# Performance work log

Measured on AMD Instinct MI355X. Metric: run time of the kernel, lower is better.

## Reference

```python
import jax, jax.numpy as jnp
import numpy as np

NA = 100000   # authors
NP_ = 100000  # papers
D = 128       # hidden dim
H = 4         # heads
DH = 32       # head dim (D = H*DH)
L = 2         # layers
R = 3         # relations: 0=writes(a->p), 1=rev_writes(p->a), 2=cites(p->p)
E = 400000    # edges per relation
OUT = 40


def setup_inputs() -> dict:
    key = jax.random.key(0)
    ks = jax.random.split(key, 16)
    s = 0.05
    return {
        "x_author": jax.random.normal(ks[0], (NA, D), jnp.float32),
        "x_paper": jax.random.normal(ks[1], (NP_, D), jnp.float32),
        "ei_writes": jax.random.randint(ks[2], (2, E), 0, NA, dtype=jnp.int32),
        "ei_rev": jax.random.randint(ks[3], (2, E), 0, NA, dtype=jnp.int32),
        "ei_cites": jax.random.randint(ks[4], (2, E), 0, NP_, dtype=jnp.int32),
        "proj_w": jax.random.normal(ks[5], (2, D, D), jnp.float32) * s,
        "proj_b": jax.random.normal(ks[6], (2, D), jnp.float32) * s,
        "kqv_w": jax.random.normal(ks[7], (L, 3, 2, D, D), jnp.float32) * s,  # [layer, {k,q,v}, type, D, D]
        "kqv_b": jax.random.normal(ks[8], (L, 3, 2, D), jnp.float32) * s,
        "out_w": jax.random.normal(ks[9], (L, 2, D, D), jnp.float32) * s,
        "out_b": jax.random.normal(ks[10], (L, 2, D), jnp.float32) * s,
        "rel_a": jax.random.normal(ks[11], (L, R, H, DH, DH), jnp.float32) * s,
        "rel_m": jax.random.normal(ks[12], (L, R, H, DH, DH), jnp.float32) * s,
        "p_rel": jnp.ones((L, R, H), jnp.float32),
        "skip": jnp.ones((L, 2), jnp.float32),
        "cls_w": jax.random.normal(ks[13], (D, OUT), jnp.float32) * s,
        "cls_b": jnp.zeros((OUT,), jnp.float32),
    }


def _seg_softmax(sc, dst, n):
    # softmax over incoming edges grouped by destination node; sc: [E,H]
    m = jax.ops.segment_max(sc, dst, num_segments=n)
    m = jnp.where(jnp.isfinite(m), m, 0.0)
    e = jnp.exp(sc - m[dst])
    z = jax.ops.segment_sum(e, dst, num_segments=n)
    return e / (z[dst] + 1e-16)


def _hgt_layer(h_a, h_p, ei_w, ei_r, ei_c, kqv_w, kqv_b, out_w, out_b, rel_a, rel_m, p_rel, skip):
    na, npp = h_a.shape[0], h_p.shape[0]

    def kqv(h, t):
        k = (h @ kqv_w[0, t] + kqv_b[0, t]).reshape(-1, H, DH)
        q = (h @ kqv_w[1, t] + kqv_b[1, t]).reshape(-1, H, DH)
        v = (h @ kqv_w[2, t] + kqv_b[2, t]).reshape(-1, H, DH)
        return k, q, v

    k_a, q_a, v_a = kqv(h_a, 0)
    k_p, q_p, v_p = kqv(h_p, 1)
    scale = 1.0 / jnp.sqrt(jnp.float32(DH))

    def edge_msgs(k_src, v_src, q_dst, ei, r):
        ke = jnp.einsum('ehd,hdf->ehf', k_src[ei[0]], rel_a[r])
        ve = jnp.einsum('ehd,hdf->ehf', v_src[ei[0]], rel_m[r])
        sc = (q_dst[ei[1]] * ke).sum(-1) * p_rel[r] * scale  # [E,H]
        return sc, ve

    # destination = paper: writes (r=0) + cites (r=2); softmax jointly per dst node
    sc_w, ve_w = edge_msgs(k_a, v_a, q_p, ei_w, 0)
    sc_c, ve_c = edge_msgs(k_p, v_p, q_p, ei_c, 2)
    sc_p = jnp.concatenate([sc_w, sc_c], 0)
    ve_p = jnp.concatenate([ve_w, ve_c], 0)
    dst_p = jnp.concatenate([ei_w[1], ei_c[1]], 0)
    al_p = _seg_softmax(sc_p, dst_p, npp)
    agg_p = jax.ops.segment_sum(ve_p * al_p[..., None], dst_p, num_segments=npp).reshape(npp, D)

    # destination = author: rev_writes (r=1)
    sc_r, ve_r = edge_msgs(k_p, v_p, q_a, ei_r, 1)
    al_a = _seg_softmax(sc_r, ei_r[1], na)
    agg_a = jax.ops.segment_sum(ve_r * al_a[..., None], ei_r[1], num_segments=na).reshape(na, D)

    def out_mix(agg, h, t):
        o = jax.nn.gelu(agg, approximate=False) @ out_w[t] + out_b[t]
        s = jax.nn.sigmoid(skip[t])
        return s * o + (1.0 - s) * h

    # HGTNet.forward applies ELU after each HGTConv (dropout is identity in eval mode)
    h_a = jax.nn.elu(out_mix(agg_a, h_a, 0))
    h_p = jax.nn.elu(out_mix(agg_p, h_p, 1))
    return h_a, h_p


def reference(x_author, x_paper, ei_writes, ei_rev, ei_cites, proj_w, proj_b,
              kqv_w, kqv_b, out_w, out_b, rel_a, rel_m, p_rel, skip, cls_w, cls_b):
    h_a = x_author @ proj_w[0] + proj_b[0]
    h_p = x_paper @ proj_w[1] + proj_b[1]
    for l in range(L):
        h_a, h_p = _hgt_layer(h_a, h_p, ei_writes, ei_rev, ei_cites,
                              kqv_w[l], kqv_b[l], out_w[l], out_b[l],
                              rel_a[l], rel_m[l], p_rel[l], skip[l])
    return h_p @ cls_w + cls_b
```

## Files before the change

### kernel.cpp

```cpp
#include <hip/hip_runtime.h>
#include <hip/hip_bf16.h>
#include <math.h>

constexpr int NA  = 100000;
constexpr int NPP = 100000;
constexpr int D   = 128;
constexpr int H   = 4;
constexpr int E   = 400000;
constexpr int R   = 3;
constexpr int L   = 2;
constexpr int NSLOT = 23;
constexpr int SLOT_ELEMS = 8 * 4 * 512;
constexpr int GB2c = (NA + 127) / 128;
constexpr int GAc  = NA / 8;
constexpr int MEGA_G = 1564 * 9;

using s8v = __attribute__((ext_vector_type(8))) short;
using f4v = __attribute__((ext_vector_type(4))) float;
typedef unsigned short ushort_t;

static __device__ __forceinline__ unsigned short f2bf(float f) {
  unsigned u = __float_as_uint(f);
  return (unsigned short)((u + 0x7fffu + ((u >> 16) & 1u)) >> 16);
}
static __device__ __forceinline__ float bf2f(unsigned short s) {
  return __uint_as_float(((unsigned)s) << 16);
}
static __device__ __forceinline__ float klo(int i) {
  return __uint_as_float(((unsigned)i) << 16);
}
static __device__ __forceinline__ float vhi(int i) {
  return __uint_as_float(((unsigned)i) & 0xffff0000u);
}
static __device__ __forceinline__ float gelu_f(float x) {
  return 0.5f * x * (1.0f + erff(x * 0.70710678118654752f));
}
static __device__ __forceinline__ float elu_f(float x) {
  return x > 0.0f ? x : expm1f(x);
}

static __device__ __forceinline__ void load_a2(
    const ushort_t* __restrict__ A, int ar0, int ar1, int ks, int g,
    s8v& a0, s8v& a1) {
  const ushort_t* ap0 = A + (size_t)ar0 * 128 + ks * 32 + g * 4;
  ushort4 u0 = *(const ushort4*)ap0;
  ushort4 u1 = *(const ushort4*)(ap0 + 16);
  a0[0]=(short)u0.x; a0[1]=(short)u0.y; a0[2]=(short)u0.z; a0[3]=(short)u0.w;
  a0[4]=(short)u1.x; a0[5]=(short)u1.y; a0[6]=(short)u1.z; a0[7]=(short)u1.w;
  const ushort_t* ap1 = A + (size_t)ar1 * 128 + ks * 32 + g * 4;
  ushort4 v0 = *(const ushort4*)ap1;
  ushort4 v1 = *(const ushort4*)(ap1 + 16);
  a1[0]=(short)v0.x; a1[1]=(short)v0.y; a1[2]=(short)v0.z; a1[3]=(short)v0.w;
  a1[4]=(short)v1.x; a1[5]=(short)v1.y; a1[6]=(short)v1.z; a1[7]=(short)v1.w;
}

template<bool GELU_A, bool MIX>
__device__ __forceinline__ void dev_gemm8(
    const ushort_t* __restrict__ A, const ushort_t* __restrict__ Bhi,
    const float* __restrict__ bias, ushort_t* __restrict__ Cout,
    const float* __restrict__ skip_ptr, int M, int bx, ushort_t* Bs) {
  for (int i = threadIdx.x; i < 2048; i += 256)
    *(s8v*)&Bs[i * 8] = *(const s8v*)(Bhi + (size_t)i * 8);
  __syncthreads();
  const int lane = threadIdx.x & 63;
  const int wave = threadIdx.x >> 6;
  const int row0 = bx * 128 + wave * 32;
  const int g = lane >> 4, li = lane & 15;
  f4v acc0[8], acc1[8];
#pragma unroll
  for (int ct = 0; ct < 8; ++ct) {
    acc0[ct] = f4v{0.f, 0.f, 0.f, 0.f};
    acc1[ct] = f4v{0.f, 0.f, 0.f, 0.f};
  }
  int ar0 = row0 + li;       if (ar0 >= M) ar0 = M - 1;
  int ar1 = row0 + 16 + li;  if (ar1 >= M) ar1 = M - 1;
#pragma unroll
  for (int ks = 0; ks < 4; ++ks) {
    s8v a0, a1;
    load_a2(A, ar0, ar1, ks, g, a0, a1);
    if (GELU_A) {
#pragma unroll
      for (int i = 0; i < 8; ++i) {
        a0[i] = (short)f2bf(gelu_f(bf2f((unsigned short)a0[i])));
        a1[i] = (short)f2bf(gelu_f(bf2f((unsigned short)a1[i])));
      }
    }
#pragma unroll
    for (int ct = 0; ct < 8; ++ct) {
      s8v bhi = *(const s8v*)&Bs[(ct * 4 + ks) * 512 + lane * 8];
      acc0[ct] = __builtin_amdgcn_mfma_f32_16x16x32_bf16(a0, bhi, acc0[ct], 0, 0, 0);
      acc1[ct] = __builtin_amdgcn_mfma_f32_16x16x32_bf16(a1, bhi, acc1[ct], 0, 0, 0);
    }
  }
  float sskip = 0.f;
  if (MIX) sskip = 1.f / (1.f + __expf(-*skip_ptr));
#pragma unroll
  for (int rf = 0; rf < 2; ++rf) {
#pragma unroll
    for (int ct = 0; ct < 8; ++ct) {
      int col = ct * 16 + li;
      float bv = bias[col];
      f4v a = rf ? acc1[ct] : acc0[ct];
#pragma unroll
      for (int r = 0; r < 4; ++r) {
        int grow = row0 + rf * 16 + g * 4 + r;
        if (grow < M) {
          float v = a[r] + bv;
          size_t off = (size_t)grow * 128 + col;
          if constexpr (MIX) {
            float hprev = bf2f(Cout[off]);
            Cout[off] = f2bf(elu_f(sskip * v + (1.f - sskip) * hprev));
          } else {
            Cout[off] = f2bf(v);
          }
        }
      }
    }
  }
}

__device__ __forceinline__ void dev_gemm_kv(
    const ushort_t* __restrict__ A, const ushort_t* __restrict__ Bkv,
    const float* __restrict__ bias, ushort_t* __restrict__ kvout,
    int M, int bx, int ch, ushort_t* Bs) {
  for (int i = threadIdx.x; i < 2048; i += 256) {
    int kvh = i >> 10, j = i & 1023;
    const ushort_t* src = Bkv + (size_t)kvh * SLOT_ELEMS + ch * 8192 + j * 8;
    *(s8v*)&Bs[kvh * 8192 + j * 8] = *(const s8v*)src;
  }
  __syncthreads();
  const int lane = threadIdx.x & 63;
  const int wave = threadIdx.x >> 6;
  const int row0 = bx * 128 + wave * 32;
  const int g = lane >> 4, li = lane & 15;
  f4v acc0[8], acc1[8];
#pragma unroll
  for (int t = 0; t < 8; ++t) {
    acc0[t] = f4v{0.f, 0.f, 0.f, 0.f};
    acc1[t] = f4v{0.f, 0.f, 0.f, 0.f};
  }
  int ar0 = row0 + li;       if (ar0 >= M) ar0 = M - 1;
  int ar1 = row0 + 16 + li;  if (ar1 >= M) ar1 = M - 1;
#pragma unroll
  for (int ks = 0; ks < 4; ++ks) {
    s8v a0, a1;
    load_a2(A, ar0, ar1, ks, g, a0, a1);
#pragma unroll
    for (int t = 0; t < 4; ++t) {
      s8v kh = *(const s8v*)&Bs[(t * 4 + ks) * 512 + lane * 8];
      acc0[t] = __builtin_amdgcn_mfma_f32_16x16x32_bf16(a0, kh, acc0[t], 0, 0, 0);
      acc1[t] = __builtin_amdgcn_mfma_f32_16x16x32_bf16(a1, kh, acc1[t], 0, 0, 0);
      s8v vh = *(const s8v*)&Bs[8192 + (t * 4 + ks) * 512 + lane * 8];
      acc0[4 + t] = __builtin_amdgcn_mfma_f32_16x16x32_bf16(a0, vh, acc0[4 + t], 0, 0, 0);
      acc1[4 + t] = __builtin_amdgcn_mfma_f32_16x16x32_bf16(a1, vh, acc1[4 + t], 0, 0, 0);
    }
  }
#pragma unroll
  for (int rf = 0; rf < 2; ++rf) {
#pragma unroll
    for (int t = 0; t < 4; ++t) {
      int col = ch * 64 + t * 16 + li;
      float bk = bias[col], bv = bias[128 + col];
#pragma unroll
      for (int r = 0; r < 4; ++r) {
        int grow = row0 + rf * 16 + g * 4 + r;
        if (grow < M) {
          float kvl = rf ? acc1[t][r] : acc0[t][r];
          float vvl = rf ? acc1[4 + t][r] : acc0[4 + t][r];
          ushort2 o;
          o.x = f2bf(kvl + bk);
          o.y = f2bf(vvl + bv);
          *(ushort2*)(kvout + (size_t)grow * 256 + 2 * col) = o;
        }
      }
    }
  }
}

template<bool TWO>
__device__ __forceinline__ void dev_attn(
    const int* __restrict__ rp1, const int* __restrict__ col1,
    const ushort_t* __restrict__ kv1,
    const int* __restrict__ rp2, const int* __restrict__ col2,
    const ushort_t* __restrict__ kv2,
    const ushort_t* __restrict__ q,
    const float* __restrict__ prel1, const float* __restrict__ prel2,
    ushort_t* __restrict__ aggout, int ablk) {
  int lane = threadIdx.x & 63;
  int wave = threadIdx.x >> 6;
  int half = lane >> 5;
  int l32  = lane & 31;
  int dst  = ablk * 8 + wave * 2 + half;
  int head = l32 >> 3;
  const float scale = 0.17677669529663688f;
  float pr1 = prel1[head] * scale;
  float pr2 = TWO ? prel2[head] * scale : pr1;
  ushort4 qv = *(const ushort4*)(q + (size_t)dst * D + l32 * 4);
  float q0 = bf2f(qv.x), q1 = bf2f(qv.y), q2 = bf2f(qv.z), q3 = bf2f(qv.w);
  int e0a = rp1[dst];
  int d1  = rp1[dst + 1] - e0a;
  int e0b = 0, dt = d1;
  if (TWO) { e0b = rp2[dst]; dt = d1 + (rp2[dst + 1] - e0b); }
  float z = 0.f, a0 = 0.f, a1 = 0.f, a2 = 0.f, a3 = 0.f;
  for (int jj = 0; jj < dt; jj += 4) {
    int4 us[4]; bool vs[4]; float prs[4];
#pragma unroll
    for (int s2 = 0; s2 < 4; ++s2) {
      int idx = jj + s2;
      bool v = idx < dt;
      bool f = (!TWO) || (idx < d1);
      int ci = 0;
      if (v) ci = f ? (e0a + idx) : (e0b + idx - d1);
      int src = f ? col1[ci] : col2[ci];
      const ushort_t* kvp = f ? kv1 : kv2;
      us[s2] = *(const int4*)(kvp + (size_t)src * 256 + l32 * 8);
      vs[s2] = v;
      prs[s2] = f ? pr1 : pr2;
    }
#pragma unroll
    for (int s2 = 0; s2 < 4; ++s2) {
      float p = q0 * klo(us[s2].x) + q1 * klo(us[s2].y)
              + q2 * klo(us[s2].z) + q3 * klo(us[s2].w);
      p += __shfl_xor(p, 1);
      p += __shfl_xor(p, 2);
      p += __shfl_xor(p, 4);
      float e = vs[s2] ? __expf(p * prs[s2]) : 0.f;
      z  += e;
      a0 += e * vhi(us[s2].x);
      a1 += e * vhi(us[s2].y);
      a2 += e * vhi(us[s2].z);
      a3 += e * vhi(us[s2].w);
    }
  }
  float inv = 1.f / (z + 1e-16f);
  ushort4 o;
  o.x = f2bf(a0 * inv);
  o.y = f2bf(a1 * inv);
  o.z = f2bf(a2 * inv);
  o.w = f2bf(a3 * inv);
  *(ushort4*)(aggout + (size_t)dst * D + l32 * 4) = o;
}

__global__ __launch_bounds__(256, 8) void attn_p(
    const int* __restrict__ rp1, const int* __restrict__ col1,
    const ushort_t* __restrict__ kv1,
    const int* __restrict__ rp2, const int* __restrict__ col2,
    const ushort_t* __restrict__ kv2,
    const ushort_t* __restrict__ q,
    const float* __restrict__ prel1, const float* __restrict__ prel2,
    ushort_t* __restrict__ aggout) {
  dev_attn<true>(rp1, col1, kv1, rp2, col2, kv2, q, prel1, prel2, aggout, blockIdx.x);
}

__global__ __launch_bounds__(256, 4) void mega0(
    const int* __restrict__ rp_r, const int* __restrict__ col_r,
    const ushort_t* __restrict__ kv1, const ushort_t* __restrict__ q,
    const float* __restrict__ prelR, ushort_t* __restrict__ aggout,
    const ushort_t* __restrict__ h_a, const ushort_t* __restrict__ Bkv0,
    const float* __restrict__ cb0, ushort_t* __restrict__ kv2out) {
  __shared__ ushort_t Bs[16384];
  unsigned gidx = blockIdx.x;
  if (gidx % 9 == 0) {
    int gb = gidx / 9;
    dev_gemm_kv(h_a, Bkv0, cb0, kv2out, NA, gb >> 1, gb & 1, Bs);
  } else {
    int ablk = gidx - gidx / 9 - 1;
    if (ablk < GAc)
      dev_attn<false>(rp_r, col_r, kv1, nullptr, nullptr, nullptr,
                      q, prelR, prelR, aggout, ablk);
  }
}

__global__ __launch_bounds__(256, 4) void fusedA(
    const ushort_t* __restrict__ agg_a, const ushort_t* __restrict__ Bout,
    const float* __restrict__ out_b0, ushort_t* __restrict__ h_a,
    const float* __restrict__ skip0,
    const ushort_t* __restrict__ h_p, const ushort_t* __restrict__ Bq,
    const float* __restrict__ bq_p, ushort_t* __restrict__ qout,
    const ushort_t* __restrict__ Bkv, const float* __restrict__ cb2,
    ushort_t* __restrict__ kvout) {
  __shared__ ushort_t Bs[16384];
  if (blockIdx.y == 0) {
    dev_gemm8<true, true>(agg_a, Bout, out_b0, h_a, skip0, NA, blockIdx.x, Bs);
  } else if (blockIdx.y == 1) {
    dev_gemm8<false, false>(h_p, Bq, bq_p, qout, nullptr, NPP, blockIdx.x, Bs);
  } else {
    dev_gemm_kv(h_p, Bkv, cb2, kvout, NPP, blockIdx.x, blockIdx.y - 2, Bs);
  }
}

__global__ __launch_bounds__(256, 4) void gemm_qkv(
    const ushort_t* __restrict__ Aq, const ushort_t* __restrict__ Akv,
    const ushort_t* __restrict__ Bq, const ushort_t* __restrict__ Bkv,
    const float* __restrict__ bias_q, const float* __restrict__ bias_kv,
    ushort_t* __restrict__ qout, ushort_t* __restrict__ kvout, int M) {
  __shared__ ushort_t Bs[16384];
  if (blockIdx.y == 0)
    dev_gemm8<false, false>(Aq, Bq, bias_q, qout, nullptr, M, blockIdx.x, Bs);
  else
    dev_gemm_kv(Akv, Bkv, bias_kv, kvout, M, blockIdx.x, blockIdx.y - 1, Bs);
}

__global__ __launch_bounds__(256, 4) void outmix(
    const ushort_t* __restrict__ agg, const ushort_t* __restrict__ Bout,
    const float* __restrict__ out_b1, ushort_t* __restrict__ h,
    const float* __restrict__ skip1, int M) {
  __shared__ ushort_t Bs[16384];
  dev_gemm8<true, true>(agg, Bout, out_b1, h, skip1, M, blockIdx.x, Bs);
}

template<int NT16, int NCOLS, int STORE, bool BLO, typename TA>
__global__ __launch_bounds__(256, 4) void gemm4(
    const TA* __restrict__ A,
    const ushort_t* __restrict__ Bhi, const ushort_t* __restrict__ Blo,
    const float* __restrict__ bias, void* __restrict__ Cv, int M) {
  constexpr int HN = NT16 * 2048;
  __shared__ ushort_t Bs[HN * (BLO ? 2 : 1)];
  constexpr bool AFP32 = sizeof(TA) == 4;
  for (int i = threadIdx.x; i < (HN / 8) * (BLO ? 2 : 1); i += 256) {
    int half = i / (HN / 8), j = i % (HN / 8);
    const ushort_t* src = (half ? Blo : Bhi) + (size_t)j * 8;
    *(s8v*)&Bs[half * HN + j * 8] = *(const s8v*)src;
  }
  __syncthreads();
  const int lane = threadIdx.x & 63;
  const int wave = threadIdx.x >> 6;
  const int row0 = blockIdx.x * 128 + wave * 32;
  const int g = lane >> 4, li = lane & 15;
  f4v acc0[NT16], acc1[NT16];
#pragma unroll
  for (int ct = 0; ct < NT16; ++ct) {
    acc0[ct] = f4v{0.f, 0.f, 0.f, 0.f};
    acc1[ct] = f4v{0.f, 0.f, 0.f, 0.f};
  }
  int ar0 = row0 + li;       if (ar0 >= M) ar0 = M - 1;
  int ar1 = row0 + 16 + li;  if (ar1 >= M) ar1 = M - 1;
#pragma unroll
  for (int ks = 0; ks < 4; ++ks) {
    s8v ahi[2], alo[2];
#pragma unroll
    for (int rf = 0; rf < 2; ++rf) {
      int ar = rf ? ar1 : ar0;
      if constexpr (AFP32) {
        const float* ap = (const float*)A + (size_t)ar * 128 + ks * 32 + g * 4;
        float4 u0 = *(const float4*)ap;
        float4 u1 = *(const float4*)(ap + 16);
        float x[8] = {u0.x, u0.y, u0.z, u0.w, u1.x, u1.y, u1.z, u1.w};
#pragma unroll
        for (int i = 0; i < 8; ++i) {
          unsigned short h = f2bf(x[i]);
          ahi[rf][i] = (short)h;
          alo[rf][i] = (short)f2bf(x[i] - bf2f(h));
        }
      } else {
        const ushort_t* ap = (const ushort_t*)A + (size_t)ar * 128 + ks * 32 + g * 4;
        ushort4 u0 = *(const ushort4*)ap;
        ushort4 u1 = *(const ushort4*)(ap + 16);
        ahi[rf][0]=(short)u0.x; ahi[rf][1]=(short)u0.y; ahi[rf][2]=(short)u0.z; ahi[rf][3]=(short)u0.w;
        ahi[rf][4]=(short)u1.x; ahi[rf][5]=(short)u1.y; ahi[rf][6]=(short)u1.z; ahi[rf][7]=(short)u1.w;
      }
    }
#pragma unroll
    for (int ct = 0; ct < NT16; ++ct) {
      const ushort_t* bp = &Bs[(ct * 4 + ks) * 512 + lane * 8];
      s8v bhi = *(const s8v*)bp;
      acc0[ct] = __builtin_amdgcn_mfma_f32_16x16x32_bf16(ahi[0], bhi, acc0[ct], 0, 0, 0);
      acc1[ct] = __builtin_amdgcn_mfma_f32_16x16x32_bf16(ahi[1], bhi, acc1[ct], 0, 0, 0);
      if constexpr (BLO) {
        s8v blo = *(const s8v*)(bp + HN);
        if constexpr (AFP32) {
          acc0[ct] = __builtin_amdgcn_mfma_f32_16x16x32_bf16(alo[0], bhi, acc0[ct], 0, 0, 0);
          acc1[ct] = __builtin_amdgcn_mfma_f32_16x16x32_bf16(alo[1], bhi, acc1[ct], 0, 0, 0);
        }
        acc0[ct] = __builtin_amdgcn_mfma_f32_16x16x32_bf16(ahi[0], blo, acc0[ct], 0, 0, 0);
        acc1[ct] = __builtin_amdgcn_mfma_f32_16x16x32_bf16(ahi[1], blo, acc1[ct], 0, 0, 0);
      }
    }
  }
#pragma unroll
  for (int rf = 0; rf < 2; ++rf) {
#pragma unroll
    for (int ct = 0; ct < NT16; ++ct) {
      int col = ct * 16 + li;
      bool colok = (col < NCOLS);
      float bv = colok ? bias[col] : 0.f;
      f4v a = rf ? acc1[ct] : acc0[ct];
#pragma unroll
      for (int r = 0; r < 4; ++r) {
        int grow = row0 + rf * 16 + g * 4 + r;
        if (grow < M && colok) {
          float v = a[r] + bv;
          size_t off = (size_t)grow * NCOLS + col;
          if constexpr (STORE == 1) ((ushort_t*)Cv)[off] = f2bf(v);
          else                      ((float*)Cv)[off] = v;
        }
      }
    }
  }
}

__global__ __launch_bounds__(256) void combine_w(
    const float* __restrict__ kqv_w, const float* __restrict__ kqv_b,
    const float* __restrict__ rel_a, const float* __restrict__ rel_m,
    float* __restrict__ cw, float* __restrict__ cb) {
  int b  = blockIdx.x;
  int kv = b & 1;
  int r  = (b >> 1) % R;
  int l  = b / (2 * R);
  int t_src = (r == 0) ? 0 : 1;
  int i_w   = (kv == 0) ? 0 : 2;
  const float* W    = kqv_w + ((size_t)((l*3 + i_w)*2 + t_src)) * D * D;
  const float* bvec = kqv_b + ((size_t)((l*3 + i_w)*2 + t_src)) * D;
  const float* rel  = ((kv == 0) ? rel_a : rel_m) + ((size_t)(l*R + r)) * H * 32 * 32;
  float* Cout = cw + (size_t)b * D * D;
  float* cbo  = cb + (size_t)b * D;
  for (int idx = threadIdx.x; idx < D * D; idx += 256) {
    int i = idx / D, j = idx % D;
    int h = j >> 5, f = j & 31;
    const float* relh = rel + h * 32 * 32;
    float sum = 0.f;
#pragma unroll
    for (int d = 0; d < 32; ++d) sum += W[i*D + (h*32 + d)] * relh[d*32 + f];
    Cout[idx] = sum;
  }
  if (threadIdx.x < D) {
    int j = threadIdx.x;
    int h = j >> 5, f = j & 31;
    const float* relh = rel + h * 32 * 32;
    float sum = 0.f;
#pragma unroll
    for (int d = 0; d < 32; ++d) sum += bvec[h*32 + d] * relh[d*32 + f];
    cbo[j] = sum;
  }
}

__global__ __launch_bounds__(256) void pack_b(
    const float* __restrict__ proj_w, const float* __restrict__ kqv_w,
    const float* __restrict__ out_w, const float* __restrict__ cls_w,
    const float* __restrict__ cw,
    ushort_t* __restrict__ phi, ushort_t* __restrict__ plo) {
  int slot = blockIdx.x;
  const float* src; int ncol = 128;
  if (slot == 0) src = proj_w;
  else if (slot == 1) src = proj_w + D * D;
  else if (slot == 22) { src = cls_w; ncol = 40; }
  else {
    int l = (slot - 2) / 10, k = (slot - 2) % 10;
    if (k == 0)      src = kqv_w + ((size_t)((l*3 + 1)*2 + 0)) * D * D;
    else if (k == 1) src = kqv_w + ((size_t)((l*3 + 1)*2 + 1)) * D * D;
    else if (k < 8)  { int idx = k - 2; src = cw + ((size_t)((l*R)*2 + idx)) * D * D; }
    else             src = out_w + ((size_t)(l*2 + (k - 8))) * D * D;
  }
  int nt = (ncol + 15) / 16;
  int total = nt * 4 * 512;
  ushort_t* ph = phi + (size_t)slot * SLOT_ELEMS;
  ushort_t* pl = plo + (size_t)slot * SLOT_ELEMS;
  for (int idx = threadIdx.x; idx < total; idx += 256) {
    int j = idx & 7, lane = (idx >> 3) & 63, ks = (idx >> 9) & 3, ct = idx >> 11;
    int k = 4 * (lane >> 4) + (j & 3) + 16 * (j >> 2) + 32 * ks;
    int n = ct * 16 + (lane & 15);
    float v = (n < ncol) ? src[(size_t)k * ncol + n] : 0.f;
    unsigned short h = f2bf(v);
    ph[idx] = h;
    pl[idx] = f2bf(v - bf2f(h));
  }
}

__global__ void count3(const int* __restrict__ ei_w, const int* __restrict__ ei_c,
                       const int* __restrict__ ei_r, int* __restrict__ degz) {
  const int* dst = blockIdx.y == 0 ? ei_w + E : blockIdx.y == 1 ? ei_c + E : ei_r + E;
  int* deg = degz + blockIdx.y * NPP;
  for (int e = blockIdx.x * blockDim.x + threadIdx.x; e < E; e += gridDim.x * blockDim.x)
    atomicAdd(&deg[dst[e]], 1);
}
__global__ void fill3(const int* __restrict__ ei_w, const int* __restrict__ ei_c,
                      const int* __restrict__ ei_r,
                      const int* __restrict__ rp_w, const int* __restrict__ rp_c,
                      const int* __restrict__ rp_r,
                      int* __restrict__ cntz, int* __restrict__ colz) {
  int rel = blockIdx.y;
  const int* ei = rel == 0 ? ei_w : rel == 1 ? ei_c : ei_r;
  const int* dst = ei + E;
  const int* rp  = rel == 0 ? rp_w : rel == 1 ? rp_c : rp_r;
  int* cnt = cntz + rel * NPP;
  int* col = colz + rel * E;
  for (int e = blockIdx.x * blockDim.x + threadIdx.x; e < E; e += gridDim.x * blockDim.x) {
    int d = dst[e];
    int pos = atomicAdd(&cnt[d], 1);
    col[rp[d] + pos] = ei[e];
  }
}

__global__ __launch_bounds__(256) void scan_partial(const int* __restrict__ degz,
                                                    int* __restrict__ bsum) {
  int blk = blockIdx.x, rel = blk / 25, t25 = blk % 25;
  const int* deg = degz + rel * NPP + t25 * 4096;
  int nrem = min(4096, NPP - t25 * 4096);
  int base = threadIdx.x * 16;
  int s = 0;
  if (base < nrem) {
#pragma unroll
    for (int i4 = 0; i4 < 4; ++i4) {
      int4 v = *(const int4*)(deg + base + i4 * 4);
      s += v.x + v.y + v.z + v.w;
    }
  }
  __shared__ int sm[256];
  sm[threadIdx.x] = s; __syncthreads();
  for (int o = 128; o > 0; o >>= 1) {
    if (threadIdx.x < o) sm[threadIdx.x] += sm[threadIdx.x + o];
    __syncthreads();
  }
  if (threadIdx.x == 0) bsum[blk] = sm[0];
}
__global__ __launch_bounds__(256) void scan_final(const int* __restrict__ degz,
                                                  const int* __restrict__ bsum,
                                                  int* rp_w, int* rp_c, int* rp_r) {
  int blk = blockIdx.x, rel = blk / 25, t25 = blk % 25;
  const int* deg = degz + rel * NPP + t25 * 4096;
  int* rpb = (rel == 0 ? rp_w : rel == 1 ? rp_c : rp_r);
  int* rp = rpb + t25 * 4096;
  int boffv = 0;
  for (int i = 0; i < t25; ++i) boffv += bsum[rel * 25 + i];
  int nrem = min(4096, NPP - t25 * 4096);
  int base = threadIdx.x * 16;
  bool ok = base < nrem;
  int v[16]; int s = 0;
  if (ok) {
#pragma unroll
    for (int i4 = 0; i4 < 4; ++i4) {
      int4 u = *(const int4*)(deg + base + i4 * 4);
      v[i4*4+0] = u.x; v[i4*4+1] = u.y; v[i4*4+2] = u.z; v[i4*4+3] = u.w;
      s += u.x + u.y + u.z + u.w;
    }
  }
  __shared__ int sm[256];
  sm[threadIdx.x] = s; __syncthreads();
  for (int o = 1; o < 256; o <<= 1) {
    int x = (threadIdx.x >= o) ? sm[threadIdx.x - o] : 0;
    __syncthreads(); sm[threadIdx.x] += x; __syncthreads();
  }
  int run = boffv + sm[threadIdx.x] - s;
  if (ok) {
    int w[16];
#pragma unroll
    for (int i = 0; i < 16; ++i) { w[i] = run; run += v[i]; }
#pragma unroll
    for (int i4 = 0; i4 < 4; ++i4) *(int4*)(rp + base + i4 * 4) = *(const int4*)&w[i4*4];
  }
  if (t25 == 24 && threadIdx.x == 255) rpb[NPP] = boffv + sm[255];
}

extern "C" void kernel_launch(void* const* d_in, const int* in_sizes, int n_in,
                              void* d_out, int out_size, void* d_ws, size_t ws_size,
                              hipStream_t stream) {
  const float* x_a    = (const float*)d_in[0];
  const float* x_p    = (const float*)d_in[1];
  const int*   ei_w   = (const int*)d_in[2];
  const int*   ei_r   = (const int*)d_in[3];
  const int*   ei_c   = (const int*)d_in[4];
  const float* proj_w = (const float*)d_in[5];
  const float* proj_b = (const float*)d_in[6];
  const float* kqv_w  = (const float*)d_in[7];
  const float* kqv_b  = (const float*)d_in[8];
  const float* out_w  = (const float*)d_in[9];
  const float* out_b  = (const float*)d_in[10];
  const float* rel_a  = (const float*)d_in[11];
  const float* rel_m  = (const float*)d_in[12];
  const float* p_rel  = (const float*)d_in[13];
  const float* skip   = (const float*)d_in[14];
  const float* cls_w  = (const float*)d_in[15];
  const float* cls_b  = (const float*)d_in[16];
  float* out = (float*)d_out;

  const size_t NF = (size_t)NA * D;
  float* ws    = (float*)d_ws;
  float* cw    = ws;
  float* cb    = cw + 12 * D * D;
  ushort_t* h_a   = (ushort_t*)(cb + 12 * D);
  ushort_t* h_p   = h_a + NF;
  ushort_t* b_q   = h_p + NF;
  ushort_t* b_q2  = b_q + NF;
  ushort_t* b_kv  = b_q2 + NF;
  ushort_t* b_kv2 = b_kv + 2 * NF;
  ushort_t* phi   = b_kv2 + 2 * NF;
  ushort_t* plo   = phi + (size_t)NSLOT * SLOT_ELEMS;
  int* ip    = (int*)(plo + (size_t)NSLOT * SLOT_ELEMS);
  int* rp_w  = ip;
  int* rp_c  = rp_w + (NPP + 1);
  int* rp_r  = rp_c + (NPP + 1);
  int* degz  = rp_r + (NA + 1);
  int* cntz  = degz + 3 * NPP;
  int* colz  = cntz + 3 * NPP;
  int* bsum  = colz + 3 * E;
  size_t need_bytes = (size_t)((char*)(bsum + 128) - (char*)d_ws);
  if (ws_size < need_bytes) return;

  hipMemsetAsync(degz, 0, sizeof(int) * 6 * (size_t)NPP, stream);

  count3<<<dim3(256, 3), 256, 0, stream>>>(ei_w, ei_c, ei_r, degz);
  scan_partial<<<75, 256, 0, stream>>>(degz, bsum);
  scan_final<<<75, 256, 0, stream>>>(degz, bsum, rp_w, rp_c, rp_r);
  fill3<<<dim3(256, 3), 256, 0, stream>>>(ei_w, ei_c, ei_r, rp_w, rp_c, rp_r, cntz, colz);
  int* col_w = colz;
  int* col_c = colz + E;
  int* col_r = colz + 2 * E;

  combine_w<<<12, 256, 0, stream>>>(kqv_w, kqv_b, rel_a, rel_m, cw, cb);
  pack_b<<<NSLOT, 256, 0, stream>>>(proj_w, kqv_w, out_w, cls_w, cw, phi, plo);

  auto PH = [&](int s){ return phi + (size_t)s * SLOT_ELEMS; };
  auto PL = [&](int s){ return plo + (size_t)s * SLOT_ELEMS; };

  const dim3 G1(GB2c, 1), GQKV(GB2c, 3), GF(GB2c, 4);
  gemm4<8, 128, 1, true, float><<<G1, 256, 0, stream>>>(
      x_a, PH(0), PL(0), proj_b,     h_a, NA);
  gemm4<8, 128, 1, true, float><<<G1, 256, 0, stream>>>(
      x_p, PH(1), PL(1), proj_b + D, h_p, NPP);

  for (int l = 0; l < L; ++l) {
    const int SQA = 2 + l * 10 + 0, SQP = 2 + l * 10 + 1;
    auto SKV = [&](int r){ return 2 + l * 10 + 2 + r * 2; };
    const int SO0 = 2 + l * 10 + 8, SO1 = 2 + l * 10 + 9;
    const float* bq_a = kqv_b + ((size_t)((l*3 + 1)*2 + 0)) * D;
    const float* bq_p = kqv_b + ((size_t)((l*3 + 1)*2 + 1)) * D;
    auto CB2 = [&](int r){ return cb + ((size_t)((l*R + r)*2)) * D; };
    const float* prelW = p_rel + (size_t)(l*R + 0) * H;
    const float* prelR = p_rel + (size_t)(l*R + 1) * H;
    const float* prelC = p_rel + (size_t)(l*R + 2) * H;

    gemm_qkv<<<GQKV, 256, 0, stream>>>(
        h_a, h_p, PH(SQA), PH(SKV(1)), bq_a, CB2(1), b_q, b_kv, NA);
    mega0<<<MEGA_G, 256, 0, stream>>>(
        rp_r, col_r, b_kv, b_q, prelR, b_q,
        h_a, PH(SKV(0)), CB2(0), b_kv2);
    fusedA<<<GF, 256, 0, stream>>>(
        b_q, PH(SO0), out_b + (size_t)(l*2 + 0) * D, h_a, skip + l*2 + 0,
        h_p, PH(SQP), bq_p, b_q2,
        PH(SKV(2)), CB2(2), b_kv);
    attn_p<<<GAc, 256, 0, stream>>>(
        rp_w, col_w, b_kv2, rp_c, col_c, b_kv,
        b_q2, prelW, prelC, b_q2);
    outmix<<<G1, 256, 0, stream>>>(
        b_q2, PH(SO1), out_b + (size_t)(l*2 + 1) * D, h_p, skip + l*2 + 1, NPP);
  }

  gemm4<3, 40, 0, true, ushort_t><<<G1, 256, 0, stream>>>(
      h_p, PH(22), PL(22), cls_b, out, NPP);
}
```

Before: 875.8 us.

## Merge per-layer stages into three wide kernels using a third KV buffer

When the workspace can hold a third K/V buffer, each layer runs three launches instead of five. One grid computes all Q and KV projections for both node types, one interleaves author and paper attention blocks, and one runs both output-mix GEMMs. The goal is to cut launch and tail-serialization overhead and to give each launch more independent blocks so the GPU stays full. This costs extra workspace memory, and mixing different block types in one grid may unbalance scheduling. The old five-launch path remains as a fallback when the workspace is too small.

```diff
diff --git a/kernel.cpp b/kernel.cpp
--- a/kernel.cpp
+++ b/kernel.cpp
@@ -241,6 +241,56 @@
   *(ushort4*)(aggout + (size_t)dst * D + l32 * 4) = o;
 }
 
+__global__ __launch_bounds__(256, 4) void biggemm(
+    const ushort_t* __restrict__ h_a, const ushort_t* __restrict__ h_p,
+    const ushort_t* __restrict__ Bqa, const ushort_t* __restrict__ Bqp,
+    const ushort_t* __restrict__ BkvR, const ushort_t* __restrict__ BkvW,
+    const ushort_t* __restrict__ BkvC,
+    const float* __restrict__ bqa, const float* __restrict__ bqp,
+    const float* __restrict__ cbR, const float* __restrict__ cbW,
+    const float* __restrict__ cbC,
+    ushort_t* __restrict__ b_q, ushort_t* __restrict__ b_q2,
+    ushort_t* __restrict__ kvR, ushort_t* __restrict__ kvW,
+    ushort_t* __restrict__ kvC) {
+  __shared__ ushort_t Bs[16384];
+  int y = blockIdx.y;
+  if (y == 0)      dev_gemm8<false, false>(h_a, Bqa, bqa, b_q,  nullptr, NA,  blockIdx.x, Bs);
+  else if (y == 1) dev_gemm8<false, false>(h_p, Bqp, bqp, b_q2, nullptr, NPP, blockIdx.x, Bs);
+  else if (y <= 3) dev_gemm_kv(h_p, BkvR, cbR, kvR, NPP, blockIdx.x, y - 2, Bs);
+  else if (y <= 5) dev_gemm_kv(h_a, BkvW, cbW, kvW, NA,  blockIdx.x, y - 4, Bs);
+  else             dev_gemm_kv(h_p, BkvC, cbC, kvC, NPP, blockIdx.x, y - 6, Bs);
+}
+
+__global__ __launch_bounds__(256, 8) void bigattn(
+    const int* __restrict__ rp_r, const int* __restrict__ col_r,
+    const ushort_t* __restrict__ kvR, ushort_t* __restrict__ q_a,
+    const int* __restrict__ rp_w, const int* __restrict__ col_w,
+    const ushort_t* __restrict__ kvW,
+    const int* __restrict__ rp_c, const int* __restrict__ col_c,
+    const ushort_t* __restrict__ kvC, ushort_t* __restrict__ q_p,
+    const float* __restrict__ prelR, const float* __restrict__ prelW,
+    const float* __restrict__ prelC) {
+  unsigned x = blockIdx.x;
+  if (x & 1)
+    dev_attn<false>(rp_r, col_r, kvR, nullptr, nullptr, nullptr,
+                    q_a, prelR, prelR, q_a, (int)(x >> 1));
+  else
+    dev_attn<true>(rp_w, col_w, kvW, rp_c, col_c, kvC,
+                   q_p, prelW, prelC, q_p, (int)(x >> 1));
+}
+
+__global__ __launch_bounds__(256, 4) void bigmix(
+    const ushort_t* __restrict__ agg_a, const ushort_t* __restrict__ Bo0,
+    const float* __restrict__ ob0, ushort_t* __restrict__ h_a,
+    const float* __restrict__ sk0,
+    const ushort_t* __restrict__ agg_p, const ushort_t* __restrict__ Bo1,
+    const float* __restrict__ ob1, ushort_t* __restrict__ h_p,
+    const float* __restrict__ sk1) {
+  __shared__ ushort_t Bs[16384];
+  if (blockIdx.y == 0) dev_gemm8<true, true>(agg_a, Bo0, ob0, h_a, sk0, NA,  blockIdx.x, Bs);
+  else                 dev_gemm8<true, true>(agg_p, Bo1, ob1, h_p, sk1, NPP, blockIdx.x, Bs);
+}
+
 __global__ __launch_bounds__(256, 8) void attn_p(
     const int* __restrict__ rp1, const int* __restrict__ col1,
     const ushort_t* __restrict__ kv1,
@@ -574,27 +624,33 @@
   float* out = (float*)d_out;
 
   const size_t NF = (size_t)NA * D;
-  float* ws    = (float*)d_ws;
-  float* cw    = ws;
-  float* cb    = cw + 12 * D * D;
-  ushort_t* h_a   = (ushort_t*)(cb + 12 * D);
-  ushort_t* h_p   = h_a + NF;
-  ushort_t* b_q   = h_p + NF;
-  ushort_t* b_q2  = b_q + NF;
-  ushort_t* b_kv  = b_q2 + NF;
-  ushort_t* b_kv2 = b_kv + 2 * NF;
-  ushort_t* phi   = b_kv2 + 2 * NF;
-  ushort_t* plo   = phi + (size_t)NSLOT * SLOT_ELEMS;
-  int* ip    = (int*)(plo + (size_t)NSLOT * SLOT_ELEMS);
-  int* rp_w  = ip;
-  int* rp_c  = rp_w + (NPP + 1);
-  int* rp_r  = rp_c + (NPP + 1);
-  int* degz  = rp_r + (NA + 1);
-  int* cntz  = degz + 3 * NPP;
-  int* colz  = cntz + 3 * NPP;
-  int* bsum  = colz + 3 * E;
-  size_t need_bytes = (size_t)((char*)(bsum + 128) - (char*)d_ws);
-  if (ws_size < need_bytes) return;
+  const size_t head_b = (size_t)(12 * D * D + 12 * D) * 4 + 4 * NF * 2;
+  const size_t kv_b   = 2 * NF * 2;
+  const size_t rest_b = 2 * (size_t)NSLOT * SLOT_ELEMS * 2 +
+                        sizeof(int) * ((size_t)3 * (NPP + 1) + 6 * NPP + 3 * E + 128);
+  const bool use3 = ws_size >= head_b + 3 * kv_b + rest_b;
+  if (!use3 && ws_size < head_b + 2 * kv_b + rest_b) return;
+
+  char* p = (char*)d_ws;
+  float* cw = (float*)p;              p += (size_t)12 * D * D * 4;
+  float* cb = (float*)p;              p += (size_t)12 * D * 4;
+  ushort_t* h_a   = (ushort_t*)p;     p += NF * 2;
+  ushort_t* h_p   = (ushort_t*)p;     p += NF * 2;
+  ushort_t* b_q   = (ushort_t*)p;     p += NF * 2;
+  ushort_t* b_q2  = (ushort_t*)p;     p += NF * 2;
+  ushort_t* b_kvR = (ushort_t*)p;     p += 2 * NF * 2;
+  ushort_t* b_kvW = (ushort_t*)p;     p += 2 * NF * 2;
+  ushort_t* b_kvC = nullptr;
+  if (use3) { b_kvC = (ushort_t*)p;   p += 2 * NF * 2; }
+  ushort_t* phi = (ushort_t*)p;       p += (size_t)NSLOT * SLOT_ELEMS * 2;
+  ushort_t* plo = (ushort_t*)p;       p += (size_t)NSLOT * SLOT_ELEMS * 2;
+  int* rp_w = (int*)p;                p += (NPP + 1) * 4;
+  int* rp_c = (int*)p;                p += (NPP + 1) * 4;
+  int* rp_r = (int*)p;                p += (NA + 1) * 4;
+  int* degz = (int*)p;                p += (size_t)3 * NPP * 4;
+  int* cntz = (int*)p;                p += (size_t)3 * NPP * 4;
+  int* colz = (int*)p;                p += (size_t)3 * E * 4;
+  int* bsum = (int*)p;
 
   hipMemsetAsync(degz, 0, sizeof(int) * 6 * (size_t)NPP, stream);
 
@@ -612,7 +668,7 @@
   auto PH = [&](int s){ return phi + (size_t)s * SLOT_ELEMS; };
   auto PL = [&](int s){ return plo + (size_t)s * SLOT_ELEMS; };
 
-  const dim3 G1(GB2c, 1), GQKV(GB2c, 3), GF(GB2c, 4);
+  const dim3 G1(GB2c, 1);
   gemm4<8, 128, 1, true, float><<<G1, 256, 0, stream>>>(
       x_a, PH(0), PL(0), proj_b,     h_a, NA);
   gemm4<8, 128, 1, true, float><<<G1, 256, 0, stream>>>(
@@ -629,20 +685,34 @@
     const float* prelR = p_rel + (size_t)(l*R + 1) * H;
     const float* prelC = p_rel + (size_t)(l*R + 2) * H;
 
-    gemm_qkv<<<GQKV, 256, 0, stream>>>(
-        h_a, h_p, PH(SQA), PH(SKV(1)), bq_a, CB2(1), b_q, b_kv, NA);
-    mega0<<<MEGA_G, 256, 0, stream>>>(
-        rp_r, col_r, b_kv, b_q, prelR, b_q,
-        h_a, PH(SKV(0)), CB2(0), b_kv2);
-    fusedA<<<GF, 256, 0, stream>>>(
-        b_q, PH(SO0), out_b + (size_t)(l*2 + 0) * D, h_a, skip + l*2 + 0,
-        h_p, PH(SQP), bq_p, b_q2,
-        PH(SKV(2)), CB2(2), b_kv);
-    attn_p<<<GAc, 256, 0, stream>>>(
-        rp_w, col_w, b_kv2, rp_c, col_c, b_kv,
-        b_q2, prelW, prelC, b_q2);
-    outmix<<<G1, 256, 0, stream>>>(
-        b_q2, PH(SO1), out_b + (size_t)(l*2 + 1) * D, h_p, skip + l*2 + 1, NPP);
+    if (use3) {
+      biggemm<<<dim3(GB2c, 8), 256, 0, stream>>>(
+          h_a, h_p, PH(SQA), PH(SQP), PH(SKV(1)), PH(SKV(0)), PH(SKV(2)),
+          bq_a, bq_p, CB2(1), CB2(0), CB2(2),
+          b_q, b_q2, b_kvR, b_kvW, b_kvC);
+      bigattn<<<2 * GAc, 256, 0, stream>>>(
+          rp_r, col_r, b_kvR, b_q,
+          rp_w, col_w, b_kvW, rp_c, col_c, b_kvC, b_q2,
+          prelR, prelW, prelC);
+      bigmix<<<dim3(GB2c, 2), 256, 0, stream>>>(
+          b_q,  PH(SO0), out_b + (size_t)(l*2 + 0) * D, h_a, skip + l*2 + 0,
+          b_q2, PH(SO1), out_b + (size_t)(l*2 + 1) * D, h_p, skip + l*2 + 1);
+    } else {
+      gemm_qkv<<<dim3(GB2c, 3), 256, 0, stream>>>(
+          h_a, h_p, PH(SQA), PH(SKV(1)), bq_a, CB2(1), b_q, b_kvR, NA);
+      mega0<<<MEGA_G, 256, 0, stream>>>(
+          rp_r, col_r, b_kvR, b_q, prelR, b_q,
+          h_a, PH(SKV(0)), CB2(0), b_kvW);
+      fusedA<<<dim3(GB2c, 4), 256, 0, stream>>>(
+          b_q, PH(SO0), out_b + (size_t)(l*2 + 0) * D, h_a, skip + l*2 + 0,
+          h_p, PH(SQP), bq_p, b_q2,
+          PH(SKV(2)), CB2(2), b_kvR);
+      attn_p<<<GAc, 256, 0, stream>>>(
+          rp_w, col_w, b_kvW, rp_c, col_c, b_kvR,
+          b_q2, prelW, prelC, b_q2);
+      outmix<<<G1, 256, 0, stream>>>(
+          b_q2, PH(SO1), out_b + (size_t)(l*2 + 1) * D, h_p, skip + l*2 + 1, NPP);
+    }
   }
 
   gemm4<3, 40, 0, true, ushort_t><<<G1, 256, 0, stream>>>(
```

Result: no change. 865.2 us (-1.2%).
